# Optimization experiments

Measured on AMD Instinct MI355X. Metric: run time of the kernel, lower is better.

The kernel has to match this reference:

```python
import jax, jax.numpy as jnp
import numpy as np

P, Q = 8, 8  # patch_size


def _patchify(x):
    # x: [b, c, H, W] -> patches [b, h*w, c*p*q]
    b, c, H, W = x.shape
    h, w = H // P, W // Q
    x = x.reshape(b, c, h, P, w, Q)
    x = x.transpose(0, 2, 4, 1, 3, 5)  # b h w c p q
    return x.reshape(b, h * w, c * P * Q)


def _depatchify(patches, c, H, W):
    # patches: [b, h*w, c*p*q] -> [b, c, H, W]
    b = patches.shape[0]
    h, w = H // P, W // Q
    x = patches.reshape(b, h, w, c, P, Q)
    x = x.transpose(0, 3, 1, 4, 2, 5)  # b c h p w q
    return x.reshape(b, c, H, W)


def setup_inputs() -> dict:
    key = jax.random.key(0)
    x = jax.random.normal(key, (16, 3, 512, 512), dtype=jnp.float32)
    return {"x": x, "rank": 32}


def reference(x, rank):
    b, c, H, W = x.shape
    patches = _patchify(x)  # [b, N, D] with N = (H/8)*(W/8), D = c*64
    u, s, vt = jnp.linalg.svd(patches, full_matrices=False)
    u = u[..., :rank]          # [b, N, r]
    s = s[..., :rank]          # [b, r]
    vt = vt[..., :rank, :]     # [b, r, D]
    # original: u*sqrt(s), v = sqrt(s)*vt^T; reconstruction u @ v^T == (u*s) @ vt
    recon = (u * s[..., None, :]) @ vt  # [b, N, D]
    return _depatchify(recon, c, H, W)
```

## Files before the change

kernel.cpp:

```cpp
#include <hip/hip_runtime.h>
#include <cstdint>
#include <cstddef>

#define IMG 512
#define JD 192

__device__ inline float fast_rcp(float x) { return __builtin_amdgcn_rcpf(x); }

__global__ __launch_bounds__(512) void k_gram(const float* __restrict__ x,
                                              float* __restrict__ part) {
  const int ck = blockIdx.x;
  const int sl = blockIdx.y;
  const int b  = blockIdx.z;
  const int t  = threadIdx.x;
  __shared__ float tile[2][32][JD];
  __shared__ float pacc[256*37];
  const int g   = t >> 8;
  const int tid = t & 255;
  const int ty = tid >> 5;
  const int tx = tid & 31;
  const int r0 = sl*48 + ty*6;
  const int c0 = tx*6;
  float acc[6][6];
#pragma unroll
  for (int i=0;i<6;i++)
#pragma unroll
    for (int j=0;j<6;j++) acc[i][j]=0.f;
  const float* xb = x + (size_t)b*3*IMG*IMG;
  const int nbeg = ck*1024;
  const int nlo = g*16, nhi = nlo+16;

  int snl[3]; size_t cpo[3]; float* wp0[3];
#pragma unroll
  for (int k=0;k<3;k++) {
    const int f = t + k*512;
    const int nl = f/48, j4 = f - nl*48;
    const int c = j4 >> 4, p = (j4 >> 1) & 7, q = (j4 & 1)*4;
    snl[k] = nl;
    cpo[k] = (size_t)(c*IMG + p)*IMG + q;
    wp0[k] = &tile[0][nl][j4*4];
  }
  float4 regs[3];
#pragma unroll
  for (int k=0;k<3;k++) {
    const int n = nbeg + snl[k];
    regs[k] = *(const float4*)(xb + cpo[k] + (size_t)(n>>6)*8*IMG + (n&63)*8);
  }
#pragma unroll
  for (int k=0;k<3;k++) *(float4*)wp0[k] = regs[k];
  __syncthreads();

  int cur = 0;
  for (int it=0; it<32; it++) {
    if (it < 31) {
      const int n0 = nbeg + (it+1)*32;
#pragma unroll
      for (int k=0;k<3;k++) {
        const int n = n0 + snl[k];
        regs[k] = *(const float4*)(xb + cpo[k] + (size_t)(n>>6)*8*IMG + (n&63)*8);
      }
    }
    const float* tb = &tile[cur][0][0];
#pragma unroll 4
    for (int nl = nlo; nl < nhi; nl++) {
      const float* tr = tb + nl*JD;
      const float2 a01 = *(const float2*)(tr + r0);
      const float2 a23 = *(const float2*)(tr + r0+2);
      const float2 a45 = *(const float2*)(tr + r0+4);
      const float2 b01 = *(const float2*)(tr + c0);
      const float2 b23 = *(const float2*)(tr + c0+2);
      const float2 b45 = *(const float2*)(tr + c0+4);
      const float va[6] = {a01.x,a01.y,a23.x,a23.y,a45.x,a45.y};
      const float vb[6] = {b01.x,b01.y,b23.x,b23.y,b45.x,b45.y};
#pragma unroll
      for (int i=0;i<6;i++)
#pragma unroll
        for (int j=0;j<6;j++) acc[i][j] += va[i]*vb[j];
    }
    if (it < 31) {
#pragma unroll
      for (int k=0;k<3;k++) *(float4*)(wp0[k] + (cur^1)*6144) = regs[k];
    }
    __syncthreads();
    cur ^= 1;
  }
  if (g == 1) {
#pragma unroll
    for (int i=0;i<6;i++)
#pragma unroll
      for (int j=0;j<6;j++) pacc[tid*37 + i*6+j] = acc[i][j];
  }
  __syncthreads();
  if (g == 0) {
    float* dst = part + (((size_t)(b*4 + sl))*4 + ck) * (size_t)(48*JD);
#pragma unroll
    for (int i=0;i<6;i++)
#pragma unroll
      for (int j=0;j<6;j++)
        dst[(ty*6+i)*JD + c0+j] = acc[i][j] + pacc[tid*37 + i*6+j];
  }
}

__global__ __launch_bounds__(256) void k_greduce(const float* __restrict__ part,
                                                 float* __restrict__ Gs) {
  const int idx = blockIdx.x*256 + threadIdx.x;
  const int b = idx / (JD*JD);
  const int e = idx - b*(JD*JD);
  const int r = e / JD;
  const int sl = r / 48;
  const int w = (r - sl*48)*JD + (e - r*JD);
  const float* p = part + ((size_t)(b*4+sl))*4*(48*JD) + w;
  float s = 0.f;
#pragma unroll
  for (int ck=0; ck<4; ck++) s += p[(size_t)ck*48*JD];
  Gs[idx] = s * (1.0f/4096.0f);
}

__global__ __launch_bounds__(256) void k_sq(const float* __restrict__ S,
                                            float* __restrict__ D) {
  const int tp = blockIdx.x;
  const int b  = blockIdx.y;
  int ti, tj;
  if      (tp==0){ti=0;tj=0;} else if (tp==1){ti=1;tj=0;}
  else if (tp==2){ti=1;tj=1;} else if (tp==3){ti=2;tj=0;}
  else if (tp==4){ti=2;tj=1;} else            {ti=2;tj=2;}
  const float* Sb = S + (size_t)b*JD*JD;
  float* Db = D + (size_t)b*JD*JD;
  __shared__ float Ar[64][33];
  __shared__ float Br[64][33];
  const int t = threadIdx.x;
  const int ty = t >> 4, tx = t & 15;
  float acc[4][4];
#pragma unroll
  for (int i=0;i<4;i++)
#pragma unroll
    for (int j=0;j<4;j++) acc[i][j]=0.f;
  for (int k0=0; k0<JD; k0+=32) {
    for (int f=t; f<2048; f+=256) {
      const int row = f >> 5, kk = f & 31;
      Ar[row][kk] = Sb[(ti*64+row)*JD + k0+kk];
      Br[row][kk] = Sb[(tj*64+row)*JD + k0+kk];
    }
    __syncthreads();
#pragma unroll 4
    for (int k=0;k<32;k++) {
      float va[4], vb[4];
#pragma unroll
      for (int i=0;i<4;i++) va[i] = Ar[ty*4+i][k];
#pragma unroll
      for (int j=0;j<4;j++) vb[j] = Br[tx*4+j][k];
#pragma unroll
      for (int i=0;i<4;i++)
#pragma unroll
        for (int j=0;j<4;j++) acc[i][j] += va[i]*vb[j];
    }
    __syncthreads();
  }
#pragma unroll
  for (int i=0;i<4;i++)
#pragma unroll
    for (int j=0;j<4;j++) {
      const int r = ti*64+ty*4+i, c = tj*64+tx*4+j;
      Db[r*JD+c] = acc[i][j];
      if (ti != tj) Db[c*JD+r] = acc[i][j];
    }
}


__device__ void orth_lds(float* __restrict__ Wl, float* __restrict__ Wpart,
                         float* __restrict__ S1,
                         float* __restrict__ rdv, float* __restrict__ pdv,
                         float* __restrict__ misc, int t, float ridge) {
  const int g = t >> 8;
  const int tid = t & 255;
  const int ty = tid >> 4, tx = tid & 15;
  float acc[4][4];
#pragma unroll
  for (int i=0;i<4;i++)
#pragma unroll
    for (int j=0;j<4;j++) acc[i][j]=0.f;
  __syncthreads();
  {
    const int rbeg = g*96;
#pragma unroll 2
    for (int r=rbeg; r<rbeg+96; r++) {
      const float4 va4 = *(const float4*)(Wl + r*68 + ty*4);
      const float4 vb4 = *(const float4*)(Wl + r*68 + tx*4);
      const float a4[4] = {va4.x, va4.y, va4.z, va4.w};
      const float b4[4] = {vb4.x, vb4.y, vb4.z, vb4.w};
#pragma unroll
      for (int i=0;i<4;i++)
#pragma unroll
        for (int j=0;j<4;j++) acc[i][j] += a4[i]*b4[j];
    }
  }
  if (g == 1) {
#pragma unroll
    for (int i=0;i<4;i++)
#pragma unroll
      for (int j=0;j<4;j++)
        Wpart[(ty*4+i)*68 + tx*4+j] = acc[i][j];
  }
  __syncthreads();
  if (g == 0) {
#pragma unroll
    for (int i=0;i<4;i++)
#pragma unroll
      for (int j=0;j<4;j++)
        S1[(ty*4+i)*68 + tx*4+j] = acc[i][j] + Wpart[(ty*4+i)*68 + tx*4+j];
  }
  __syncthreads();
  if (ridge > 0.f) {
    if (t < 64) {
      float d = S1[t*68+t];
#pragma unroll
      for (int o=1;o<64;o<<=1) d = fmaxf(d, __shfl_xor(d, o));
      if (t == 0) misc[0] = d * ridge;
    }
    __syncthreads();
    if (t < 64) S1[t*68+t] += misc[0];
    __syncthreads();
  }
  for (int p=0; p<4; p++) {
    const int b16 = p*16;
    if (t < 64) {
      for (int jj=0; jj<16; jj++) {
        const int j = b16 + jj;
        const float invd = fast_rcp(S1[j*68+j]);
        if (t == 0) pdv[jj] = invd;
        const int nit = (15-jj)*16;
        for (int f=t; f<nit; f+=64) {
          const int i = j+1 + (f>>4);
          const int k = j+1 + (f&15);
          if (k <= i)
            S1[i*68+k] -= S1[i*68+j]*S1[k*68+j]*invd;
        }
      }
    }
    __syncthreads();
    const int rb = b16 + 16;
    if (t < 64 - rb) {
      const int r = rb + t;
      float pr[16];
      float4* prp = (float4*)pr;
      prp[0] = *(const float4*)(S1 + r*68 + b16);
      prp[1] = *(const float4*)(S1 + r*68 + b16 + 4);
      prp[2] = *(const float4*)(S1 + r*68 + b16 + 8);
      prp[3] = *(const float4*)(S1 + r*68 + b16 + 12);
#pragma unroll
      for (int c=1; c<16; c++) {
        float s = pr[c];
#pragma unroll
        for (int j=0; j<c; j++) s -= pr[j]*S1[(b16+c)*68 + b16+j]*pdv[j];
        pr[c] = s;
      }
      *(float4*)(S1 + r*68 + b16)      = prp[0];
      *(float4*)(S1 + r*68 + b16 + 4)  = prp[1];
      *(float4*)(S1 + r*68 + b16 + 8)  = prp[2];
      *(float4*)(S1 + r*68 + b16 + 12) = prp[3];
    }
    __syncthreads();
    for (int f=t; f<2304; f+=512) {
      const int i = rb + f/48;
      const int k = rb + (f - (f/48)*48);
      if (i < 64 && k < 64 && k <= i) {
        float s = S1[i*68+k];
#pragma unroll
        for (int jj=0; jj<16; jj++)
          s -= S1[i*68 + b16+jj]*S1[k*68 + b16+jj]*pdv[jj];
        S1[i*68+k] = s;
      }
    }
    __syncthreads();
  }
  if (t < 64) rdv[t] = rsqrtf(S1[t*68+t]);
  __syncthreads();
  for (int f=t; f<4096; f+=512) {
    const int i = f>>6, k = f&63;
    if (k < i) S1[i*68+k] *= rdv[k];
  }
  __syncthreads();
  if (t < JD) {
    float w[64];
    float4* wp = (float4*)w;
#pragma unroll
    for (int c4=0;c4<16;c4++) wp[c4] = *(const float4*)(Wl + t*68 + c4*4);
#pragma unroll
    for (int c=0;c<64;c++) {
      float v = w[c];
#pragma unroll
      for (int k=0;k<c;k++) v -= w[k]*S1[c*68+k];
      w[c] = v * rdv[c];
    }
#pragma unroll
    for (int c4=0;c4<16;c4++) *(float4*)(Wl + t*68 + c4*4) = wp[c4];
  }
  __syncthreads();
}

__device__ void mm_lds(const float* __restrict__ G, const float* __restrict__ Win,
                       float* __restrict__ Wout, float* __restrict__ Gt, int t) {
  const int rg = t >> 3;
  const int cg = t & 7;
  float acc[4][8];
#pragma unroll
  for (int i=0;i<4;i++)
#pragma unroll
    for (int j=0;j<8;j++) acc[i][j]=0.f;
  for (int k0=0; k0<JD; k0+=32) {
    __syncthreads();
    for (int f=t; f<6144; f+=512) {
      const int kk = f / 192, r = f - kk*192;
      Gt[kk*196 + r] = G[r*JD + k0 + kk];
    }
    __syncthreads();
    if (t < 384) {
#pragma unroll 2
      for (int k=0;k<32;k++) {
        const float4 g4 = *(const float4*)(Gt + k*196 + rg*4);
        const float* wr = Win + (k0+k)*68 + cg*8;
        const float4 w0 = *(const float4*)(wr);
        const float4 w1 = *(const float4*)(wr + 4);
        const float ga[4] = {g4.x, g4.y, g4.z, g4.w};
        const float wb[8] = {w0.x,w0.y,w0.z,w0.w,w1.x,w1.y,w1.z,w1.w};
#pragma unroll
        for (int i=0;i<4;i++)
#pragma unroll
          for (int j=0;j<8;j++) acc[i][j] += ga[i]*wb[j];
      }
    }
  }
  __syncthreads();
  if (t < 384) {
#pragma unroll
    for (int i=0;i<4;i++)
#pragma unroll
      for (int j=0;j<8;j++)
        Wout[(rg*4+i)*68 + cg*8 + j] = acc[i][j];
  }
  __syncthreads();
}

__device__ void hgemm_lds(const float* __restrict__ X, const float* __restrict__ Y,
                          float* __restrict__ S1, int ss, int t) {
  const int ty = t >> 5, tx = t & 31;
  float acc[4][2];
#pragma unroll
  for (int i=0;i<4;i++)
#pragma unroll
    for (int j=0;j<2;j++) acc[i][j]=0.f;
#pragma unroll 2
  for (int r=0; r<JD; r++) {
    const float4 va4 = *(const float4*)(X + r*68 + ty*4);
    const float2 vb2 = *(const float2*)(Y + r*68 + tx*2);
    const float a4[4] = {va4.x, va4.y, va4.z, va4.w};
    const float b2[2] = {vb2.x, vb2.y};
#pragma unroll
    for (int i=0;i<4;i++)
#pragma unroll
      for (int j=0;j<2;j++) acc[i][j] += a4[i]*b2[j];
  }
  __syncthreads();
#pragma unroll
  for (int i=0;i<4;i++)
#pragma unroll
    for (int j=0;j<2;j++)
      S1[(ty*4+i)*ss + tx*2+j] = acc[i][j];
  __syncthreads();
}

__global__ __launch_bounds__(512) void k_subH(const float* __restrict__ G32g,
                                              const float* __restrict__ Gsg,
                                              float* __restrict__ WbG,
                                              float* __restrict__ Hgg) {
  const int b = blockIdx.x;
  const int t = threadIdx.x;
  __shared__ __align__(16) float W0l[192*68];
  __shared__ __align__(16) float W1l[192*68];
  __shared__ __align__(16) float scr[32*196];
  __shared__ float rdv[64];
  __shared__ float pdv[16];
  __shared__ float misc[8];
  const float* Gb  = G32g + (size_t)b*JD*JD;
  const float* Gsb = Gsg  + (size_t)b*JD*JD;

  for (int f=t; f<JD*64; f+=512)
    W0l[(f>>6)*68 + (f&63)] = Gb[(f>>6)*JD + (f&63)];
  __syncthreads();

  orth_lds(W0l, W1l, scr, rdv, pdv, misc, t, 1e-6f);
  mm_lds(Gb, W0l, W1l, scr, t);
  orth_lds(W1l, W0l, scr, rdv, pdv, misc, t, 1e-6f);
  orth_lds(W1l, W0l, scr, rdv, pdv, misc, t, 0.f);

  mm_lds(Gsb, W1l, W0l, scr, t);
  hgemm_lds(W1l, W0l, scr, 65, t);

  float* Wb = WbG + (size_t)b*JD*64;
  for (int f=t; f<JD*64; f+=512)
    Wb[f] = W1l[(f>>6)*68 + (f&63)];
  float* Hb = Hgg + (size_t)b*4160;
  for (int f=t; f<4160; f+=512) Hb[f] = scr[f];
}

__device__ void dev_tridiag(float* __restrict__ A, float* a, float* b2,
                            float* bsg, float* v0s, float* bts,
                            float* vvec, float* wvec, int t) {
  for (int j=0; j<=61; j++) {
    const int m = 63 - j;
    if (t < 64) {
      float xi = (t < m) ? A[j*65 + (j+1+t)] : 0.f;
      float nr = xi*xi;
#pragma unroll
      for (int o=1;o<64;o<<=1) nr += __shfl_xor(nr, o);
      const float sig = sqrtf(nr);
      const float alpha = __shfl(xi, 0);
      const float sgn = (alpha >= 0.f) ? 1.f : -1.f;
      const float v0 = alpha + sgn*sig;
      const float beta = (sig > 1e-20f) ? 1.0f/(sig*fabsf(v0)) : 0.f;
      if (t < m) vvec[t] = (t==0) ? v0 : xi;
      if (t == 0) {
        a[j] = A[j*65+j]; b2[j] = nr; bsg[j] = -sgn*sig;
        v0s[j] = v0; bts[j] = beta;
      }
      float pv = 0.f;
      if (t < m) {
        const float* row = A + (j+1+t)*65 + (j+1);
        for (int c=0;c<m;c++) pv += row[c]*vvec[c];
        pv *= beta;
      }
      float dp = (t<m) ? vvec[t]*pv : 0.f;
#pragma unroll
      for (int o=1;o<64;o<<=1) dp += __shfl_xor(dp, o);
      const float gamma = 0.5f*beta*dp;
      if (t < m) wvec[t] = pv - gamma*vvec[t];
    }
    __syncthreads();
    const int mm = m*m;
    for (int f=t; f<mm; f+=256) {
      const int r = f/m, c = f - r*m;
      A[(j+1+r)*65 + (j+1+c)] -= vvec[r]*wvec[c] + wvec[r]*vvec[c];
    }
    __syncthreads();
  }
  if (t == 0) {
    a[62] = A[62*65+62];
    a[63] = A[63*65+63];
    const float bb = A[62*65+63];
    b2[62] = bb*bb;
    bsg[62] = bb;
  }
  __syncthreads();
}

__device__ inline int sturm_cnt_fast(const float* a, const float* b2, float sig) {
  float d = a[0] - sig;
  int n = (d < 0.f) ? 1 : 0;
#pragma unroll 8
  for (int i=1;i<64;i++) {
    const float dd = (fabsf(d) < 1e-20f) ? -1e-20f : d;
    d = (a[i]-sig) - b2[i-1]*fast_rcp(dd);
    n += (d < 0.f) ? 1 : 0;
  }
  return n;
}

__device__ inline float dguard(float d) {
  if (fabsf(d) < 1e-12f) return (d < 0.f) ? -1e-12f : 1e-12f;
  return d;
}

__global__ __launch_bounds__(256) void k_eigv(const float* __restrict__ Hgg,
                                              float* __restrict__ VtG) {
  const int b = blockIdx.x;
  const int t = threadIdx.x;
  __shared__ float SH[4160];
  __shared__ float Vt[64*36];
  __shared__ float dpA[64*33];
  __shared__ float dmA[64*33];
  __shared__ float ps[8*33];
  __shared__ float wvred[32];
  __shared__ float rdv[64];
  __shared__ float a64[64];
  __shared__ float b2v[64];
  __shared__ float bsg[64];
  __shared__ float v0s[64];
  __shared__ float bts[64];
  __shared__ float vvec[64];
  __shared__ float wvec[64];
  __shared__ float lam[32];
  __shared__ float misc[8];
  const float* Hb = Hgg + (size_t)b*4160;
  for (int f=t; f<4160; f+=256) SH[f] = Hb[f];
  __syncthreads();

  dev_tridiag(SH, a64, b2v, bsg, v0s, bts, vvec, wvec, t);

  if (t < 64) {
    const float bl = (t>0)  ? sqrtf(b2v[t-1]) : 0.f;
    const float br = (t<63) ? sqrtf(b2v[t])   : 0.f;
    float lo = a64[t] - bl - br, hi = a64[t] + bl + br;
#pragma unroll
    for (int o=1;o<64;o<<=1) {
      lo = fminf(lo, __shfl_xor(lo,o));
      hi = fmaxf(hi, __shfl_xor(hi,o));
    }
    if (t == 0) { misc[0] = lo - 1e-4f; misc[1] = hi + 1e-4f; }
  }
  __syncthreads();

  {
    const int l = t >> 3, g = t & 7;
    const int r = 32 + l;
    float L = misc[0], H = misc[1];
    for (int it=0; it<10; it++) {
      const float mid = L + (H-L)*((float)(g+1)*(1.0f/9.0f));
      const int cnt = sturm_cnt_fast(a64, b2v, mid);
      float nL = L, nH = H;
#pragma unroll
      for (int k=0;k<8;k++) {
        const int ck = __shfl(cnt, k, 8);
        const float pk = L + (H-L)*((float)(k+1)*(1.0f/9.0f));
        if (ck <= r) nL = fmaxf(nL, pk); else nH = fminf(nH, pk);
      }
      L = nL; H = nH;
    }
    if (g == 0) lam[l] = 0.5f*(L+H);
  }
  __syncthreads();

  if (t < 32) {
    const int l = t;
    const float lm = lam[l];
    float d = dguard(a64[0] - lm);
    dpA[0*33+l] = d;
    for (int i=1;i<64;i++) {
      d = dguard((a64[i]-lm) - b2v[i-1]*fast_rcp(d));
      dpA[i*33+l] = d;
    }
    float e = dguard(a64[63] - lm);
    dmA[63*33+l] = e;
    for (int i=62;i>=0;i--) {
      e = dguard((a64[i]-lm) - b2v[i]*fast_rcp(e));
      dmA[i*33+l] = e;
    }
    int ks = 0; float gbest = 1e30f;
    for (int i=0;i<64;i++) {
      const float g = fabsf(dpA[i*33+l] + dmA[i*33+l] - (a64[i]-lm));
      if (g < gbest) { gbest = g; ks = i; }
    }
    Vt[ks*36+l] = 1.f;
    float z = 1.f;
    for (int i=ks-1;i>=0;i--) {
      z = -(bsg[i]*z) * fast_rcp(dpA[i*33+l]);
      z = fminf(fmaxf(z, -1e18f), 1e18f);
      Vt[i*36+l] = z;
    }
    z = 1.f;
    for (int i=ks+1;i<64;i++) {
      z = -(bsg[i-1]*z) * fast_rcp(dmA[i*33+l]);
      z = fminf(fmaxf(z, -1e18f), 1e18f);
      Vt[i*36+l] = z;
    }
    float nr2 = 0.f;
    for (int i=0;i<64;i++) { const float zz = Vt[i*36+l]; nr2 += zz*zz; }
    const float inv = rsqrtf(nr2);
    for (int i=0;i<64;i++) Vt[i*36+l] *= inv;
  }
  __syncthreads();

  for (int f=t; f<1024; f+=256) {
    const int i = f>>5, j = f&31;
    float s = 0.f;
    for (int r=0;r<64;r++) s += Vt[r*36+i]*Vt[r*36+j];
    dpA[i*33+j] = s;
  }
  __syncthreads();
  if (t == 0) {
    float m = 0.f;
    for (int j=0;j<32;j++) m = fmaxf(m, dpA[j*33+j]);
    misc[2] = m * 1e-7f;
  }
  __syncthreads();
  if (t < 32) dpA[t*33+t] += misc[2];
  for (int j=0;j<31;j++) {
    __syncthreads();
    const float invd = fast_rcp(dpA[j*33+j]);
    for (int f=t; f<(31-j)*32; f+=256) {
      const int i = j+1 + (f>>5);
      const int k = f & 31;
      if (k > j && k <= i)
        dpA[i*33+k] -= dpA[i*33+j]*dpA[k*33+j]*invd;
    }
  }
  __syncthreads();
  if (t < 32) rdv[t] = rsqrtf(dpA[t*33+t]);
  __syncthreads();
  for (int f=t; f<1024; f+=256) {
    const int i = f>>5, k = f&31;
    if (k < i) dpA[i*33+k] *= rdv[k];
  }
  __syncthreads();
  if (t < 64) {
    float w[32];
#pragma unroll
    for (int c=0;c<32;c++) w[c] = Vt[t*36+c];
#pragma unroll
    for (int c=0;c<32;c++) {
      float v = w[c];
#pragma unroll
      for (int k=0;k<c;k++) v -= w[k]*dpA[c*33+k];
      w[c] = v * rdv[c];
    }
#pragma unroll
    for (int c=0;c<32;c++) Vt[t*36+c] = w[c];
  }
  __syncthreads();

  for (int j=61; j>=0; j--) {
    const int m = 63 - j;
    {
      const int c = t & 31, g = t >> 5;
      float s = 0.f;
      for (int r=g; r<m; r+=8) {
        const float vr = (r==0) ? v0s[j] : SH[j*65 + (j+1+r)];
        s += vr * Vt[(j+1+r)*36 + c];
      }
      ps[g*33+c] = s;
    }
    __syncthreads();
    if (t < 32) {
      float s = 0.f;
#pragma unroll
      for (int g=0;g<8;g++) s += ps[g*33+t];
      wvred[t] = s * bts[j];
    }
    __syncthreads();
    {
      const int c = t & 31, g = t >> 5;
      for (int r=g; r<m; r+=8) {
        const float vr = (r==0) ? v0s[j] : SH[j*65 + (j+1+r)];
        Vt[(j+1+r)*36 + c] -= vr * wvred[c];
      }
    }
    __syncthreads();
  }

  float* Vb = VtG + (size_t)b*2048;
  for (int f=t; f<2048; f+=256) Vb[f] = Vt[(f>>5)*36 + (f&31)];
}

__global__ __launch_bounds__(256) void k_bv(const float* __restrict__ WbG,
                                            const float* __restrict__ VtG,
                                            float* __restrict__ Btg) {
  const int b = blockIdx.x;
  const int t = threadIdx.x;
  __shared__ float Vt[64*36];
  const float* W = WbG + (size_t)b*JD*64;
  const float* Vb = VtG + (size_t)b*2048;
  float* Bt = Btg + (size_t)b*32*JD;
  for (int f=t; f<2048; f+=256) Vt[(f>>5)*36 + (f&31)] = Vb[f];
  __syncthreads();
  if (t < JD) {
    float accv[32];
#pragma unroll
    for (int c=0;c<32;c++) accv[c] = 0.f;
    const float4* crow = (const float4*)(W + t*64);
#pragma unroll 2
    for (int kb=0; kb<16; kb++) {
      const float4 av = crow[kb];
      const float a4[4] = {av.x, av.y, av.z, av.w};
#pragma unroll
      for (int ki=0; ki<4; ki++) {
        const float aa = a4[ki];
        const float* vrow = Vt + (kb*4+ki)*36;
        const float4 v0 = *(const float4*)(vrow+0);
        const float4 v1 = *(const float4*)(vrow+4);
        const float4 v2 = *(const float4*)(vrow+8);
        const float4 v3 = *(const float4*)(vrow+12);
        const float4 v4 = *(const float4*)(vrow+16);
        const float4 v5 = *(const float4*)(vrow+20);
        const float4 v6 = *(const float4*)(vrow+24);
        const float4 v7 = *(const float4*)(vrow+28);
        accv[0]+=aa*v0.x; accv[1]+=aa*v0.y; accv[2]+=aa*v0.z; accv[3]+=aa*v0.w;
        accv[4]+=aa*v1.x; accv[5]+=aa*v1.y; accv[6]+=aa*v1.z; accv[7]+=aa*v1.w;
        accv[8]+=aa*v2.x; accv[9]+=aa*v2.y; accv[10]+=aa*v2.z; accv[11]+=aa*v2.w;
        accv[12]+=aa*v3.x; accv[13]+=aa*v3.y; accv[14]+=aa*v3.z; accv[15]+=aa*v3.w;
        accv[16]+=aa*v4.x; accv[17]+=aa*v4.y; accv[18]+=aa*v4.z; accv[19]+=aa*v4.w;
        accv[20]+=aa*v5.x; accv[21]+=aa*v5.y; accv[22]+=aa*v5.z; accv[23]+=aa*v5.w;
        accv[24]+=aa*v6.x; accv[25]+=aa*v6.y; accv[26]+=aa*v6.z; accv[27]+=aa*v6.w;
        accv[28]+=aa*v7.x; accv[29]+=aa*v7.y; accv[30]+=aa*v7.z; accv[31]+=aa*v7.w;
      }
    }
#pragma unroll
    for (int c=0;c<32;c++) Bt[c*JD + t] = accv[c];
  }
}

__global__ __launch_bounds__(256) void k_mm(const float* __restrict__ Btg,
                                            float* __restrict__ Mg) {
  const int tp = blockIdx.x;
  const int b  = blockIdx.y;
  int ti, tj;
  if      (tp==0){ti=0;tj=0;} else if (tp==1){ti=1;tj=0;}
  else if (tp==2){ti=1;tj=1;} else if (tp==3){ti=2;tj=0;}
  else if (tp==4){ti=2;tj=1;} else            {ti=2;tj=2;}
  const float* Bt = Btg + (size_t)b*32*JD;
  float* Mb = Mg + (size_t)b*JD*JD;
  __shared__ float Ar[32][68];
  __shared__ float Br[32][68];
  const int t = threadIdx.x;
  const int ty = t >> 4, tx = t & 15;
  for (int f=t; f<2048; f+=256) {
    const int k = f >> 6, c = f & 63;
    Ar[k][c] = Bt[k*JD + ti*64 + c];
    Br[k][c] = Bt[k*JD + tj*64 + c];
  }
  __syncthreads();
  float acc[4][4];
#pragma unroll
  for (int i=0;i<4;i++)
#pragma unroll
    for (int j=0;j<4;j++) acc[i][j]=0.f;
#pragma unroll 4
  for (int k=0;k<32;k++) {
    const float4 va4 = *(const float4*)(&Ar[k][ty*4]);
    const float4 vb4 = *(const float4*)(&Br[k][tx*4]);
    const float a4[4] = {va4.x, va4.y, va4.z, va4.w};
    const float b4[4] = {vb4.x, vb4.y, vb4.z, vb4.w};
#pragma unroll
    for (int i=0;i<4;i++)
#pragma unroll
      for (int j=0;j<4;j++) acc[i][j] += a4[i]*b4[j];
  }
#pragma unroll
  for (int i=0;i<4;i++)
#pragma unroll
    for (int j=0;j<4;j++) {
      const int r = ti*64+ty*4+i, c = tj*64+tx*4+j;
      Mb[r*JD+c] = acc[i][j];
      if (ti != tj) Mb[c*JD+r] = acc[i][j];
    }
}

__global__ __launch_bounds__(256) void k_recon(const float* __restrict__ x,
                                               const float* __restrict__ Mg,
                                               float* __restrict__ out) {
  const int nb = blockIdx.x;
  const int b  = blockIdx.y;
  const int t  = threadIdx.x;
  __shared__ float At[32][17];
  __shared__ float Mt[16][JD];
  const float* xb = x + (size_t)b*3*IMG*IMG;
  const float* Mb = Mg + (size_t)b*JD*JD;
  float* ob = out + (size_t)b*3*IMG*IMG;
  const int pg = t >> 4;
  const int jg = t & 15;
  float acc[2][12];
#pragma unroll
  for (int i=0;i<2;i++)
#pragma unroll
    for (int j=0;j<12;j++) acc[i][j]=0.f;
  for (int j0=0; j0<JD; j0+=16) {
    for (int f=t; f<512; f+=256) {
      const int nl = f >> 4, jj = f & 15;
      const int j = j0 + jj;
      const int n = nb*32 + nl;
      const int hh = n >> 6, ww = n & 63;
      const int c = j >> 6, p = (j >> 3) & 7, q = j & 7;
      At[nl][jj] = xb[(c*IMG + hh*8+p)*IMG + ww*8 + q];
    }
    for (int f=t; f<768; f+=256) {
      const int jj = f/48, cc = (f - jj*48)*4;
      *(float4*)(&Mt[jj][cc]) = *(const float4*)(Mb + (size_t)(j0+jj)*JD + cc);
    }
    __syncthreads();
#pragma unroll 4
    for (int jj=0;jj<16;jj++) {
      const float a0 = At[pg*2+0][jj];
      const float a1 = At[pg*2+1][jj];
      const float4 m0 = *(const float4*)(&Mt[jj][jg*12]);
      const float4 m1 = *(const float4*)(&Mt[jj][jg*12+4]);
      const float4 m2 = *(const float4*)(&Mt[jj][jg*12+8]);
      const float mm[12] = {m0.x,m0.y,m0.z,m0.w,m1.x,m1.y,m1.z,m1.w,
                            m2.x,m2.y,m2.z,m2.w};
#pragma unroll
      for (int j=0;j<12;j++) {
        acc[0][j] += a0*mm[j];
        acc[1][j] += a1*mm[j];
      }
    }
    __syncthreads();
  }
#pragma unroll
  for (int i=0;i<2;i++) {
    const int n = nb*32 + pg*2 + i;
    const int hh = n >> 6, ww = n & 63;
#pragma unroll
    for (int j4=0;j4<3;j4++) {
      const int jo = jg*12 + j4*4;
      const int c = jo >> 6, p = (jo >> 3) & 7, q = jo & 7;
      const float4 v = make_float4(acc[i][j4*4+0], acc[i][j4*4+1],
                                   acc[i][j4*4+2], acc[i][j4*4+3]);
      *(float4*)(ob + (size_t)(c*IMG + hh*8+p)*IMG + ww*8 + q) = v;
    }
  }
}

extern "C" void kernel_launch(void* const* d_in, const int* in_sizes, int n_in,
                              void* d_out, int out_size, void* d_ws, size_t ws_size,
                              hipStream_t stream) {
  (void)in_sizes; (void)n_in; (void)out_size; (void)ws_size;
  const float* x = (const float*)d_in[0];
  float* out = (float*)d_out;
  float* ws  = (float*)d_ws;

  float* part = ws;
  float* Gs   = ws + 2359296;
  float* P0   = ws + 2949120;
  float* P1   = ws + 3538944;
  float* Mg   = ws;
  float* Wb   = ws + 786432;
  float* Hg   = ws + 983040;
  float* Vtg  = ws + 1057792;
  float* Btg  = ws + 1090560;

  k_gram  <<<dim3(4,4,16), 512, 0, stream>>>(x, part);
  k_greduce<<<2304,        256, 0, stream>>>(part, Gs);
  k_sq    <<<dim3(6,16),   256, 0, stream>>>(Gs, P0);
  k_sq    <<<dim3(6,16),   256, 0, stream>>>(P0, P1);
  k_sq    <<<dim3(6,16),   256, 0, stream>>>(P1, P0);
  k_sq    <<<dim3(6,16),   256, 0, stream>>>(P0, P1);
  k_sq    <<<dim3(6,16),   256, 0, stream>>>(P1, P0);
  k_subH  <<<16,           512, 0, stream>>>(P0, Gs, Wb, Hg);
  k_eigv  <<<16,           256, 0, stream>>>(Hg, Vtg);
  k_bv    <<<16,           256, 0, stream>>>(Wb, Vtg, Btg);
  k_mm    <<<dim3(6,16),   256, 0, stream>>>(Btg, Mg);
  k_recon <<<dim3(128,16), 256, 0, stream>>>(x, Mg, out);
}
```

Measured before the change: 854.3 us.

## Double-buffer k_sq LDS tiles with float4 prefetch and fuse k_bv into k_eigv

The symmetric squaring kernel now keeps two LDS tile buffers. It prefetches the next K-slice into registers with float4 loads while computing on the current one, which halves the barriers per slice. Separately, the W*V product that was a standalone kernel now runs at the end of the eigenvector kernel, reusing its LDS V tile. This removes one launch and a global round trip of V. The LDS footprint of k_sq doubles, and k_eigv gets longer and uses more registers.

```diff
diff --git a/kernel.cpp b/kernel.cpp
--- a/kernel.cpp
+++ b/kernel.cpp
@@ -126,35 +126,61 @@
   else if (tp==4){ti=2;tj=1;} else            {ti=2;tj=2;}
   const float* Sb = S + (size_t)b*JD*JD;
   float* Db = D + (size_t)b*JD*JD;
-  __shared__ float Ar[64][33];
-  __shared__ float Br[64][33];
+  __shared__ float Ar[2][64][33];
+  __shared__ float Br[2][64][33];
   const int t = threadIdx.x;
   const int ty = t >> 4, tx = t & 15;
+  const int row0 = t >> 3,        c40 = t & 7;
+  const int row1 = (t+256) >> 3,  c41 = (t+256) & 7;
+  const float* Sa = Sb + (size_t)(ti*64)*JD;
+  const float* Sc = Sb + (size_t)(tj*64)*JD;
+  float4 ra0, ra1, rb0, rb1;
+  auto stage_write = [&](int buf) {
+    float* a0 = &Ar[buf][row0][c40*4];
+    a0[0]=ra0.x; a0[1]=ra0.y; a0[2]=ra0.z; a0[3]=ra0.w;
+    float* a1 = &Ar[buf][row1][c41*4];
+    a1[0]=ra1.x; a1[1]=ra1.y; a1[2]=ra1.z; a1[3]=ra1.w;
+    float* b0 = &Br[buf][row0][c40*4];
+    b0[0]=rb0.x; b0[1]=rb0.y; b0[2]=rb0.z; b0[3]=rb0.w;
+    float* b1 = &Br[buf][row1][c41*4];
+    b1[0]=rb1.x; b1[1]=rb1.y; b1[2]=rb1.z; b1[3]=rb1.w;
+  };
+  ra0 = *(const float4*)(Sa + (size_t)row0*JD + c40*4);
+  ra1 = *(const float4*)(Sa + (size_t)row1*JD + c41*4);
+  rb0 = *(const float4*)(Sc + (size_t)row0*JD + c40*4);
+  rb1 = *(const float4*)(Sc + (size_t)row1*JD + c41*4);
+  stage_write(0);
+  __syncthreads();
+
   float acc[4][4];
 #pragma unroll
   for (int i=0;i<4;i++)
 #pragma unroll
     for (int j=0;j<4;j++) acc[i][j]=0.f;
-  for (int k0=0; k0<JD; k0+=32) {
-    for (int f=t; f<2048; f+=256) {
-      const int row = f >> 5, kk = f & 31;
-      Ar[row][kk] = Sb[(ti*64+row)*JD + k0+kk];
-      Br[row][kk] = Sb[(tj*64+row)*JD + k0+kk];
-    }
-    __syncthreads();
+  int cur = 0;
+  for (int s=0; s<6; s++) {
+    if (s < 5) {
+      const int k0 = (s+1)*32;
+      ra0 = *(const float4*)(Sa + (size_t)row0*JD + k0 + c40*4);
+      ra1 = *(const float4*)(Sa + (size_t)row1*JD + k0 + c41*4);
+      rb0 = *(const float4*)(Sc + (size_t)row0*JD + k0 + c40*4);
+      rb1 = *(const float4*)(Sc + (size_t)row1*JD + k0 + c41*4);
+    }
 #pragma unroll 4
     for (int k=0;k<32;k++) {
       float va[4], vb[4];
 #pragma unroll
-      for (int i=0;i<4;i++) va[i] = Ar[ty*4+i][k];
-#pragma unroll
-      for (int j=0;j<4;j++) vb[j] = Br[tx*4+j][k];
+      for (int i=0;i<4;i++) va[i] = Ar[cur][ty*4+i][k];
+#pragma unroll
+      for (int j=0;j<4;j++) vb[j] = Br[cur][tx*4+j][k];
 #pragma unroll
       for (int i=0;i<4;i++)
 #pragma unroll
         for (int j=0;j<4;j++) acc[i][j] += va[i]*vb[j];
     }
-    __syncthreads();
+    if (s < 5) stage_write(cur^1);
+    __syncthreads();
+    cur ^= 1;
   }
 #pragma unroll
   for (int i=0;i<4;i++)
@@ -165,7 +191,6 @@
       if (ti != tj) Db[c*JD+r] = acc[i][j];
     }
 }
-
 
 __device__ void orth_lds(float* __restrict__ Wl, float* __restrict__ Wpart,
                          float* __restrict__ S1,
@@ -471,7 +496,8 @@
 }
 
 __global__ __launch_bounds__(256) void k_eigv(const float* __restrict__ Hgg,
-                                              float* __restrict__ VtG) {
+                                              const float* __restrict__ WbG,
+                                              float* __restrict__ Btg) {
   const int b = blockIdx.x;
   const int t = threadIdx.x;
   __shared__ float SH[4160];
@@ -646,21 +672,8 @@
     __syncthreads();
   }
 
-  float* Vb = VtG + (size_t)b*2048;
-  for (int f=t; f<2048; f+=256) Vb[f] = Vt[(f>>5)*36 + (f&31)];
-}
-
-__global__ __launch_bounds__(256) void k_bv(const float* __restrict__ WbG,
-                                            const float* __restrict__ VtG,
-                                            float* __restrict__ Btg) {
-  const int b = blockIdx.x;
-  const int t = threadIdx.x;
-  __shared__ float Vt[64*36];
   const float* W = WbG + (size_t)b*JD*64;
-  const float* Vb = VtG + (size_t)b*2048;
   float* Bt = Btg + (size_t)b*32*JD;
-  for (int f=t; f<2048; f+=256) Vt[(f>>5)*36 + (f&31)] = Vb[f];
-  __syncthreads();
   if (t < JD) {
     float accv[32];
 #pragma unroll
@@ -822,7 +835,6 @@
   float* Mg   = ws;
   float* Wb   = ws + 786432;
   float* Hg   = ws + 983040;
-  float* Vtg  = ws + 1057792;
   float* Btg  = ws + 1090560;
 
   k_gram  <<<dim3(4,4,16), 512, 0, stream>>>(x, part);
@@ -833,8 +845,7 @@
   k_sq    <<<dim3(6,16),   256, 0, stream>>>(P0, P1);
   k_sq    <<<dim3(6,16),   256, 0, stream>>>(P1, P0);
   k_subH  <<<16,           512, 0, stream>>>(P0, Gs, Wb, Hg);
-  k_eigv  <<<16,           256, 0, stream>>>(Hg, Vtg);
-  k_bv    <<<16,           256, 0, stream>>>(Wb, Vtg, Btg);
+  k_eigv  <<<16,           256, 0, stream>>>(Hg, Wb, Btg);
   k_mm    <<<dim3(6,16),   256, 0, stream>>>(Btg, Mg);
   k_recon <<<dim3(128,16), 256, 0, stream>>>(x, Mg, out);
 }
```

Result: faster. 782.9 us (-8.4%).
